# Kernel tuning notes

Hardware: AMD Instinct MI355X
Metric: run time of the kernel (lower is better)

## Reference

```python
import jax, jax.numpy as jnp
import numpy as np

T = 8192      # sequence length (scan steps)
D_IN = 1024   # input feature dim
H = 1024      # d_model (hidden size)


def setup_inputs() -> dict:
    key = jax.random.key(0)
    k1, k2, k3, k4 = jax.random.split(key, 4)
    inputs = jax.random.normal(k1, (T, D_IN), dtype=jnp.float32)
    terminations = jax.random.randint(k2, (T,), 0, 2) > 0  # bool [T]
    last_state = jnp.zeros((H,), dtype=jnp.float32)
    # GRUCell params (flax layout: input kernel with bias for all 3 gates;
    # recurrent kernel, bias only on the candidate 'n' gate).
    # Gate order within the 3H axis: [r, z, n].
    Wi = jax.random.normal(k3, (D_IN, 3 * H), dtype=jnp.float32) / np.sqrt(D_IN)
    bi = jnp.zeros((3 * H,), dtype=jnp.float32)
    Wh = jax.random.normal(k4, (H, 3 * H), dtype=jnp.float32) / np.sqrt(H)
    bhn = jnp.zeros((H,), dtype=jnp.float32)
    return {"inputs": inputs, "terminations": terminations, "last_state": last_state,
            "Wi": Wi, "bi": bi, "Wh": Wh, "bhn": bhn}


def reference(inputs, terminations, last_state, Wi, bi, Wh, bhn):
    # Precompute all input-side gate preactivations in one big GEMM: [T, 3H]
    gi_all = inputs @ Wi + bi

    def step(h, xs):
        gi, term = xs
        # reset_on_terminate: zero the carry when the episode terminated
        h = jnp.where(term, jnp.zeros_like(h), h)
        gh = h @ Wh                      # [3H], recurrent preactivations
        gi_r, gi_z, gi_n = jnp.split(gi, 3)
        gh_r, gh_z, gh_n = jnp.split(gh, 3)
        r = jax.nn.sigmoid(gi_r + gh_r)
        z = jax.nn.sigmoid(gi_z + gh_z)
        n = jnp.tanh(gi_n + r * (gh_n + bhn))
        h_new = (1.0 - z) * n + z * h    # flax GRUCell update
        # GRUout emits (new_c, (new_c, new_h)); flax GRUCell returns new_h twice
        return h_new, (h_new, h_new)

    _, (new_states, y_t) = jax.lax.scan(step, last_state, (gi_all, terminations))
    return (y_t, new_states)  # each [T, H]
```

## Files before the change

### kernel.cpp

```cpp
#include <hip/hip_runtime.h>
#include <stdint.h>

#define T_LEN 8192
#define DIN   1024
#define HD    1024
#define TH    3072
#define NB    16
#define SKINNY_MAX 160
#define KSPLIT 5

typedef __attribute__((ext_vector_type(8))) short bf16x8;
typedef __attribute__((ext_vector_type(4))) float f32x4;

__device__ __forceinline__ unsigned short f2bf(float x) {
    union { float f; unsigned u; } v; v.f = x;
    unsigned r = v.u + 0x7FFFu + ((v.u >> 16) & 1u);
    return (unsigned short)(r >> 16);
}

__device__ __forceinline__ float bf2f(unsigned short x) {
    union { unsigned u; float f; } v; v.u = ((unsigned)x) << 16;
    return v.f;
}

__device__ __forceinline__ void gld16(const void* g, void* l) {
    __builtin_amdgcn_global_load_lds(
        (const __attribute__((address_space(1))) unsigned int*)(uintptr_t)g,
        (__attribute__((address_space(3))) unsigned int*)(uintptr_t)l,
        16, 0, 0);
}

__device__ __forceinline__ float sigm(float x) { return 1.f / (1.f + __expf(-x)); }
__device__ __forceinline__ float tanh_fast(float x) { return 1.f - 2.f / (1.f + __expf(2.f * x)); }

__global__ void cast_x(const float* __restrict__ X, unsigned short* __restrict__ Xb) {
    int idx = (blockIdx.x * 256 + threadIdx.x) * 4;
    float4 v = *(const float4*)(X + idx);
    ushort4 o; o.x = f2bf(v.x); o.y = f2bf(v.y); o.z = f2bf(v.z); o.w = f2bf(v.w);
    *(ushort4*)(Xb + idx) = o;
}

__global__ void transpose_cast(const float* __restrict__ Wi, const float* __restrict__ Wh,
                               unsigned short* __restrict__ WiT, unsigned short* __restrict__ WhT) {
    const float* src = blockIdx.z ? Wh : Wi;
    unsigned short* dst = blockIdx.z ? WhT : WiT;
    int n0 = blockIdx.x * 64, k0 = blockIdx.y * 64;
    __shared__ unsigned short tile[64][65];
    int tid = threadIdx.x;
    for (int p = 0; p < 16; p++) {
        int idx = tid + p * 256;
        int kl = idx >> 6, nl = idx & 63;
        tile[kl][nl] = f2bf(src[(size_t)(k0 + kl) * TH + n0 + nl]);
    }
    __syncthreads();
    for (int p = 0; p < 16; p++) {
        int idx = tid + p * 256;
        int nl = idx >> 6, kl = idx & 63;
        dst[(size_t)(n0 + nl) * 1024 + k0 + kl] = tile[kl][nl];
    }
}

__global__ void meta_kernel(const int* __restrict__ term, const float* __restrict__ last_state,
                            int* __restrict__ pos_list, int* __restrict__ meta) {
    __shared__ int part[1024];
    __shared__ int cnt[NB];
    __shared__ int cur[NB];
    __shared__ int flag;
    int tid = threadIdx.x;
    if (tid < NB) cnt[tid] = 0;
    if (tid == 0) flag = 0;
    __syncthreads();
    int base = tid * 8;
    int mx = -1;
    for (int u = 0; u < 8; u++) {
        int t = base + u;
        int s = (t == 0 || term[t] != 0) ? t : -1;
        mx = s > mx ? s : mx;
    }
    part[tid] = mx;
    __syncthreads();
    for (int d = 1; d < 1024; d <<= 1) {
        int a = part[tid];
        int b = (tid >= d) ? part[tid - d] : -1;
        __syncthreads();
        part[tid] = a > b ? a : b;
        __syncthreads();
    }
    int run = (tid > 0) ? part[tid - 1] : -1;
    int kk[8];
    for (int u = 0; u < 8; u++) {
        int t = base + u;
        int s = (t == 0 || term[t] != 0) ? t : -1;
        run = s > run ? s : run;
        int ls = t - run;
        int k = ls < NB ? ls : NB - 1;
        kk[u] = k;
        atomicAdd(&cnt[k], 1);
    }
    if (last_state[tid] != 0.0f) atomicOr(&flag, 1);
    __syncthreads();
    if (tid == 0) {
        int off = 0;
        for (int k = 0; k < NB; k++) {
            meta[k] = cnt[k];
            meta[NB + k] = off;
            cur[k] = off;
            off += cnt[k];
        }
        meta[2 * NB] = flag;
        meta[48] = 0;
        meta[49] = 0;
    }
    __syncthreads();
    for (int u = 0; u < 8; u++) {
        int idx = atomicAdd(&cur[kk[u]], 1);
        pos_list[idx] = base + u;
    }
}

__global__ __launch_bounds__(256) void gemm_gi(const unsigned short* __restrict__ Xb,
                                               const unsigned short* __restrict__ WiT,
                                               const float* __restrict__ bi,
                                               float* __restrict__ gi) {
    __shared__ unsigned short As[128 * 32];
    __shared__ unsigned short Bs[128 * 32];
    int tid = threadIdx.x;
    int phys = blockIdx.y * gridDim.x + blockIdx.x;
    int logi = (phys & 7) * 192 + (phys >> 3);
    int m0 = (logi / 24) * 128, n0 = (logi % 24) * 128;
    int lane = tid & 63, wave = tid >> 6;
    int wm = wave & 1, wn = wave >> 1;
    int quad = lane >> 4, l16 = lane & 15;
    f32x4 acc[4][4] = {};
    for (int kb = 0; kb < 32; kb++) {
        int k0 = kb * 32;
        for (int p = 0; p < 2; p++) {
            int c = tid + p * 256;
            int row = c >> 2, cb = c & 3;
            gld16(Xb + (size_t)(m0 + row) * 1024 + k0 + cb * 8, As + c * 8);
            gld16(WiT + (size_t)(n0 + row) * 1024 + k0 + cb * 8, Bs + c * 8);
        }
        __syncthreads();
        bf16x8 af[4], bfr[4];
        for (int i = 0; i < 4; i++)
            af[i] = *(const bf16x8*)(As + (wm * 64 + i * 16 + l16) * 32 + quad * 8);
        for (int j = 0; j < 4; j++)
            bfr[j] = *(const bf16x8*)(Bs + (wn * 64 + j * 16 + l16) * 32 + quad * 8);
        for (int i = 0; i < 4; i++)
            for (int j = 0; j < 4; j++)
                acc[i][j] = __builtin_amdgcn_mfma_f32_16x16x32_bf16(af[i], bfr[j], acc[i][j], 0, 0, 0);
        __syncthreads();
    }
    for (int j = 0; j < 4; j++) {
        int col = n0 + wn * 64 + j * 16 + l16;
        float bv = bi[col];
        for (int i = 0; i < 4; i++) {
            int rbase = m0 + wm * 64 + i * 16 + quad * 4;
            for (int r = 0; r < 4; r++)
                gi[(size_t)(rbase + r) * TH + col] = acc[i][j][r] + bv;
        }
    }
}

__global__ void pass0_kernel(const float* __restrict__ gi, const float* __restrict__ bhn,
                             const float* __restrict__ last_state, const float* __restrict__ Wh,
                             const int* __restrict__ term, const int* __restrict__ pos_list,
                             const int* __restrict__ meta, float* __restrict__ out,
                             unsigned short* __restrict__ hb) {
    int S0 = meta[0];
    int b = blockIdx.x;
    if (b >= S0) return;
    int t = pos_list[meta[NB] + b];
    int tid = threadIdx.x;
    bool ls_path = (t == 0) && (term[0] == 0) && (meta[2 * NB] != 0);
    for (int u = 0; u < 4; u++) {
        int j = tid + u * 256;
        float gr = gi[(size_t)t * TH + j];
        float gz = gi[(size_t)t * TH + 1024 + j];
        float gn = gi[(size_t)t * TH + 2048 + j];
        float hp = 0.f, ghr = 0.f, ghz = 0.f, ghn = 0.f;
        if (ls_path) {
            hp = last_state[j];
            for (int k = 0; k < 1024; k++) {
                float hk = last_state[k];
                const float* w = Wh + (size_t)k * TH;
                ghr += hk * w[j]; ghz += hk * w[1024 + j]; ghn += hk * w[2048 + j];
            }
        }
        float r = sigm(gr + ghr);
        float z = sigm(gz + ghz);
        float n = tanh_fast(gn + r * (ghn + bhn[j]));
        float h = (1.f - z) * n + z * hp;
        out[(size_t)t * HD + j] = h;
        out[(size_t)(T_LEN + t) * HD + j] = h;
        hb[(size_t)t * HD + j] = f2bf(h);
    }
}

__global__ __launch_bounds__(256) void pass_gemm(const float* __restrict__ gi,
                                                 const float* __restrict__ bhn,
                                                 const unsigned short* __restrict__ WhT,
                                                 const unsigned short* __restrict__ hb,
                                                 float* __restrict__ out,
                                                 unsigned short* __restrict__ hbw,
                                                 const int* __restrict__ pos_list,
                                                 const int* __restrict__ meta, int k) {
    int S = meta[k];
    int off = meta[NB + k];
    int tid = threadIdx.x;
    int lane = tid & 63, wave = tid >> 6;
    int quad = lane >> 4, l16 = lane & 15;

    if (S <= SKINNY_MAX) {
        if (S == 0) return;
        int nrt = (S + 15) >> 4;
        int ntask = 64 * nrt;
        int gwave = ((blockIdx.y * 16 + blockIdx.x) << 2) + wave;
        int nw = gridDim.x * gridDim.y * 4;
        for (int task = gwave; task < ntask; task += nw) {
            int ct = task & 63;
            int rt = task >> 6;
            int j = ct * 16 + l16;
            int ra = rt * 16 + l16;
            ra = ra < S ? ra : S - 1;
            int t_a = pos_list[off + ra];
            const unsigned short* ap = hb + (size_t)(t_a - 1) * HD + quad * 8;
            const unsigned short* bp = WhT + (size_t)j * 1024 + quad * 8;
            f32x4 acc[3] = {};
            #pragma unroll
            for (int ks = 0; ks < 32; ks++) {
                bf16x8 a  = *(const bf16x8*)(ap + ks * 32);
                bf16x8 b0 = *(const bf16x8*)(bp + ks * 32);
                bf16x8 b1 = *(const bf16x8*)(bp + 1048576 + ks * 32);
                bf16x8 b2 = *(const bf16x8*)(bp + 2097152 + ks * 32);
                acc[0] = __builtin_amdgcn_mfma_f32_16x16x32_bf16(a, b0, acc[0], 0, 0, 0);
                acc[1] = __builtin_amdgcn_mfma_f32_16x16x32_bf16(a, b1, acc[1], 0, 0, 0);
                acc[2] = __builtin_amdgcn_mfma_f32_16x16x32_bf16(a, b2, acc[2], 0, 0, 0);
            }
            #pragma unroll
            for (int r = 0; r < 4; r++) {
                int rr = rt * 16 + quad * 4 + r;
                if (rr >= S) continue;
                int t = pos_list[off + rr];
                const float* girow = gi + (size_t)t * TH;
                float hp = out[(size_t)(t - 1) * HD + j];
                float rgt = sigm(girow[j] + acc[0][r]);
                float zgt = sigm(girow[1024 + j] + acc[1][r]);
                float ngt = tanh_fast(girow[2048 + j] + rgt * (acc[2][r] + bhn[j]));
                float hv = (1.f - zgt) * ngt + zgt * hp;
                out[(size_t)t * HD + j] = hv;
                out[(size_t)(T_LEN + t) * HD + j] = hv;
                hbw[(size_t)t * HD + j] = f2bf(hv);
            }
        }
        return;
    }

    int r0 = blockIdx.y * 64;
    if (r0 >= S) return;
    int j0 = blockIdx.x * 64;
    __shared__ unsigned short As[4 * 64 * 32];
    __shared__ unsigned short Bs[4 * 192 * 32];
    int wm = wave & 1, wn = wave >> 1;

    int arow = tid >> 2, sub = tid & 3;
    bool av = (r0 + arow) < S;
    int t_a = av ? pos_list[off + r0 + arow] : 1;
    const unsigned short* hsrc = hb + (size_t)(t_a - 1) * HD + sub * 8;

    f32x4 acc[2][6] = {};
    for (int kb = 0; kb < 8; kb++) {
        int k0 = kb * 128;
        for (int ks = 0; ks < 4; ks++) {
            int kk0 = k0 + ks * 32;
            for (int p = 0; p < 3; p++) {
                int c = tid + p * 256;
                int row = c >> 2, q = c & 3;
                int g = row >> 6, jj = row & 63;
                gld16(WhT + (size_t)(g * 1024 + j0 + jj) * 1024 + kk0 + q * 8,
                      Bs + ks * 6144 + c * 8);
            }
            gld16(hsrc + kk0, As + ks * 2048 + tid * 8);
        }
        __syncthreads();
        for (int ks = 0; ks < 4; ks++) {
            bf16x8 af[2];
            for (int i = 0; i < 2; i++)
                af[i] = *(const bf16x8*)(As + ks * 2048 + (wm * 32 + i * 16 + l16) * 32 + quad * 8);
            for (int n = 0; n < 6; n++) {
                int g = n >> 1, jh = n & 1;
                bf16x8 bv = *(const bf16x8*)(Bs + ks * 6144 + (g * 64 + wn * 32 + jh * 16 + l16) * 32 + quad * 8);
                for (int i = 0; i < 2; i++)
                    acc[i][n] = __builtin_amdgcn_mfma_f32_16x16x32_bf16(af[i], bv, acc[i][n], 0, 0, 0);
            }
        }
        __syncthreads();
    }
    for (int i = 0; i < 2; i++) {
        for (int r = 0; r < 4; r++) {
            int rr = r0 + wm * 32 + i * 16 + quad * 4 + r;
            if (rr >= S) continue;
            int t = pos_list[off + rr];
            const float* girow = gi + (size_t)t * TH;
            const float* hprow = out + (size_t)(t - 1) * HD;
            float* o1 = out + (size_t)t * HD;
            float* o2 = out + (size_t)(T_LEN + t) * HD;
            unsigned short* hbrow = hbw + (size_t)t * HD;
            for (int jh = 0; jh < 2; jh++) {
                int j = j0 + wn * 32 + jh * 16 + l16;
                float ghr = acc[i][0 + jh][r];
                float ghz = acc[i][2 + jh][r];
                float ghn = acc[i][4 + jh][r];
                float rg = sigm(girow[j] + ghr);
                float zg = sigm(girow[1024 + j] + ghz);
                float ng = tanh_fast(girow[2048 + j] + rg * (ghn + bhn[j]));
                float h = (1.f - zg) * ng + zg * hprow[j];
                o1[j] = h;
                o2[j] = h;
                hbrow[j] = f2bf(h);
            }
        }
    }
}

__global__ __launch_bounds__(256) void skinny_all(const float* __restrict__ gi,
                                                  const float* __restrict__ bhn,
                                                  const unsigned short* __restrict__ WhT,
                                                  unsigned short* __restrict__ hb,
                                                  float* __restrict__ out,
                                                  const int* __restrict__ pos_list,
                                                  const int* __restrict__ meta,
                                                  int* __restrict__ syncc) {
    int tid = threadIdx.x;
    int lane = tid & 63, wave = tid >> 6;
    int quad = lane >> 4, l16 = lane & 15;
    int gwave = (blockIdx.x << 2) + wave;
    int gen = 0;
    for (int k = KSPLIT; k <= NB - 2; k++) {
        int S = meta[k];
        if (S == 0) break;
        int off = meta[NB + k];
        int nrt = (S + 15) >> 4;
        int ntask = 64 * nrt;
        for (int task = gwave; task < ntask; task += 512) {
            int ct = task & 63;
            int rt = task >> 6;
            int j = ct * 16 + l16;
            int ra = rt * 16 + l16;
            ra = ra < S ? ra : S - 1;
            int t_a = pos_list[off + ra];
            const unsigned short* ap = hb + (size_t)(t_a - 1) * HD + quad * 8;
            const unsigned short* bp = WhT + (size_t)j * 1024 + quad * 8;
            f32x4 acc[3] = {};
            #pragma unroll
            for (int ks = 0; ks < 32; ks++) {
                bf16x8 a  = *(const bf16x8*)(ap + ks * 32);
                bf16x8 b0 = *(const bf16x8*)(bp + ks * 32);
                bf16x8 b1 = *(const bf16x8*)(bp + 1048576 + ks * 32);
                bf16x8 b2 = *(const bf16x8*)(bp + 2097152 + ks * 32);
                acc[0] = __builtin_amdgcn_mfma_f32_16x16x32_bf16(a, b0, acc[0], 0, 0, 0);
                acc[1] = __builtin_amdgcn_mfma_f32_16x16x32_bf16(a, b1, acc[1], 0, 0, 0);
                acc[2] = __builtin_amdgcn_mfma_f32_16x16x32_bf16(a, b2, acc[2], 0, 0, 0);
            }
            #pragma unroll
            for (int r = 0; r < 4; r++) {
                int rr = rt * 16 + quad * 4 + r;
                if (rr >= S) continue;
                int t = pos_list[off + rr];
                const float* girow = gi + (size_t)t * TH;
                float hp = out[(size_t)(t - 1) * HD + j];
                float rgt = sigm(girow[j] + acc[0][r]);
                float zgt = sigm(girow[1024 + j] + acc[1][r]);
                float ngt = tanh_fast(girow[2048 + j] + rgt * (acc[2][r] + bhn[j]));
                float hv = (1.f - zgt) * ngt + zgt * hp;
                out[(size_t)t * HD + j] = hv;
                out[(size_t)(T_LEN + t) * HD + j] = hv;
                hb[(size_t)t * HD + j] = f2bf(hv);
            }
        }
        if (k == NB - 2 || meta[k + 1] == 0) break;
        gen++;
        __syncthreads();
        __threadfence();
        if (tid == 0) {
            atomicAdd(syncc, 1);
            while (atomicAdd(syncc, 0) < 128 * gen)
                __builtin_amdgcn_s_sleep(4);
        }
        __syncthreads();
        __threadfence();
    }
}

__global__ __launch_bounds__(256) void tail_pll(const float* __restrict__ gi,
                                                const float* __restrict__ bhn,
                                                const unsigned short* __restrict__ WhT,
                                                const int* __restrict__ pos_list,
                                                const int* __restrict__ meta,
                                                int* __restrict__ sync,
                                                float* __restrict__ out) {
    int S = meta[NB - 1];
    if (S == 0) return;
    __shared__ int pos[T_LEN];
    __shared__ float hsh[HD];
    __shared__ float dots[192];
    int off = meta[NB + NB - 1];
    int tid = threadIdx.x;
    int j0 = blockIdx.x * 64;
    for (int i = tid; i < S; i += 256) pos[i] = pos_list[off + i];
    __syncthreads();
    if (tid == 0) {
        for (int i = 1; i < S; i++) {
            int v = pos[i], j = i - 1;
            while (j >= 0 && pos[j] > v) { pos[j + 1] = pos[j]; j--; }
            pos[j + 1] = v;
        }
    }
    __syncthreads();
    for (int s = 0; s < S; s++) {
        int t = pos[s];
        for (int u = 0; u < 4; u++)
            hsh[tid + u * 256] = out[(size_t)(t - 1) * HD + tid + u * 256];
        __syncthreads();
        if (tid < 192) {
            int g = tid >> 6, jj = tid & 63;
            int col = g * 1024 + j0 + jj;
            const unsigned short* wrow = WhT + (size_t)col * 1024;
            float acc = 0.f;
            for (int kk = 0; kk < 1024; kk += 8) {
                bf16x8 wv = *(const bf16x8*)(wrow + kk);
                f32x4 h0 = *(const f32x4*)(hsh + kk);
                f32x4 h1 = *(const f32x4*)(hsh + kk + 4);
                acc += h0[0] * bf2f((unsigned short)wv[0]) + h0[1] * bf2f((unsigned short)wv[1])
                     + h0[2] * bf2f((unsigned short)wv[2]) + h0[3] * bf2f((unsigned short)wv[3])
                     + h1[0] * bf2f((unsigned short)wv[4]) + h1[1] * bf2f((unsigned short)wv[5])
                     + h1[2] * bf2f((unsigned short)wv[6]) + h1[3] * bf2f((unsigned short)wv[7]);
            }
            dots[tid] = acc;
        }
        __syncthreads();
        if (tid < 64) {
            int j = j0 + tid;
            float rg = sigm(gi[(size_t)t * TH + j] + dots[tid]);
            float zg = sigm(gi[(size_t)t * TH + 1024 + j] + dots[64 + tid]);
            float ng = tanh_fast(gi[(size_t)t * TH + 2048 + j] + rg * (dots[128 + tid] + bhn[j]));
            float hv = (1.f - zg) * ng + zg * hsh[j];
            out[(size_t)t * HD + j] = hv;
            out[(size_t)(T_LEN + t) * HD + j] = hv;
        }
        __threadfence();
        __syncthreads();
        if (tid == 0) {
            atomicAdd(sync, 1);
            int tgt = 16 * (s + 1);
            while (atomicAdd(sync, 0) < tgt)
                __builtin_amdgcn_s_sleep(8);
        }
        __syncthreads();
        __threadfence();
    }
}

extern "C" void kernel_launch(void* const* d_in, const int* in_sizes, int n_in,
                              void* d_out, int out_size, void* d_ws, size_t ws_size,
                              hipStream_t stream) {
    const float* X          = (const float*)d_in[0];
    const int*   term       = (const int*)d_in[1];
    const float* last_state = (const float*)d_in[2];
    const float* Wi         = (const float*)d_in[3];
    const float* bi         = (const float*)d_in[4];
    const float* Wh         = (const float*)d_in[5];
    const float* bhn        = (const float*)d_in[6];
    float* out = (float*)d_out;

    char* ws = (char*)d_ws;
    float*          gi       = (float*)ws;
    unsigned short* Xb       = (unsigned short*)(ws + 100663296);
    unsigned short* hb       = Xb;
    unsigned short* WiT      = (unsigned short*)(ws + 117440512);
    unsigned short* WhT      = (unsigned short*)(ws + 123731968);
    int*            pos_list = (int*)(ws + 130023424);
    int*            meta     = (int*)(ws + 130056192);
    int*            sync_t   = meta + 48;
    int*            sync_s   = meta + 49;

    cast_x<<<dim3(8192), dim3(256), 0, stream>>>(X, Xb);
    transpose_cast<<<dim3(48, 16, 2), dim3(256), 0, stream>>>(Wi, Wh, WiT, WhT);
    meta_kernel<<<dim3(1), dim3(1024), 0, stream>>>(term, last_state, pos_list, meta);
    gemm_gi<<<dim3(24, 64), dim3(256), 0, stream>>>(Xb, WiT, bi, gi);
    pass0_kernel<<<dim3(8192), dim3(256), 0, stream>>>(gi, bhn, last_state, Wh, term, pos_list, meta, out, hb);
    for (int k = 1; k < KSPLIT; k++) {
        int rows_max = T_LEN / (k + 1);
        int gy = (rows_max + 63) / 64;
        pass_gemm<<<dim3(16, gy), dim3(256), 0, stream>>>(gi, bhn, WhT, hb, out, hb, pos_list, meta, k);
    }
    skinny_all<<<dim3(128), dim3(256), 0, stream>>>(gi, bhn, WhT, hb, out, pos_list, meta, sync_s);
    tail_pll<<<dim3(16), dim3(256), 0, stream>>>(gi, bhn, WhT, pos_list, meta, sync_t, out);
}
```

Before: 507.5 us.

## Replace grid barrier in skinny_all with per-timestep dataflow counters

Removes the grid-wide barrier between successive reset-distance levels in the persistent skinny kernel. Each wave now spins on per-timestep completion counters (placed in the WiT workspace, which is dead after the GEMM and is zeroed in pass0) until its predecessor row is fully written, then bumps counters after writing. This lets independent rows of the next level start early instead of waiting for all blocks. The gi GEMM also drops its swizzled block-to-tile mapping in favor of a plain grid mapping, which may change L2 locality.

```diff
diff --git a/kernel.cpp b/kernel.cpp
--- a/kernel.cpp
+++ b/kernel.cpp
@@ -109,7 +109,6 @@
         }
         meta[2 * NB] = flag;
         meta[48] = 0;
-        meta[49] = 0;
     }
     __syncthreads();
     for (int u = 0; u < 8; u++) {
@@ -125,9 +124,7 @@
     __shared__ unsigned short As[128 * 32];
     __shared__ unsigned short Bs[128 * 32];
     int tid = threadIdx.x;
-    int phys = blockIdx.y * gridDim.x + blockIdx.x;
-    int logi = (phys & 7) * 192 + (phys >> 3);
-    int m0 = (logi / 24) * 128, n0 = (logi % 24) * 128;
+    int m0 = blockIdx.y * 128, n0 = blockIdx.x * 128;
     int lane = tid & 63, wave = tid >> 6;
     int wm = wave & 1, wn = wave >> 1;
     int quad = lane >> 4, l16 = lane & 15;
@@ -166,7 +163,8 @@
                              const float* __restrict__ last_state, const float* __restrict__ Wh,
                              const int* __restrict__ term, const int* __restrict__ pos_list,
                              const int* __restrict__ meta, float* __restrict__ out,
-                             unsigned short* __restrict__ hb) {
+                             unsigned short* __restrict__ hb, int* __restrict__ wcnt) {
+    if (blockIdx.x < 32) wcnt[blockIdx.x * 256 + threadIdx.x] = 0;
     int S0 = meta[0];
     int b = blockIdx.x;
     if (b >= S0) return;
@@ -330,12 +328,11 @@
                                                   float* __restrict__ out,
                                                   const int* __restrict__ pos_list,
                                                   const int* __restrict__ meta,
-                                                  int* __restrict__ syncc) {
+                                                  int* __restrict__ wcnt) {
     int tid = threadIdx.x;
     int lane = tid & 63, wave = tid >> 6;
     int quad = lane >> 4, l16 = lane & 15;
     int gwave = (blockIdx.x << 2) + wave;
-    int gen = 0;
     for (int k = KSPLIT; k <= NB - 2; k++) {
         int S = meta[k];
         if (S == 0) break;
@@ -349,6 +346,15 @@
             int ra = rt * 16 + l16;
             ra = ra < S ? ra : S - 1;
             int t_a = pos_list[off + ra];
+            if (k > KSPLIT) {
+                for (;;) {
+                    int c = __hip_atomic_load(&wcnt[t_a - 1], __ATOMIC_RELAXED,
+                                              __HIP_MEMORY_SCOPE_AGENT);
+                    if (__all(c >= 64)) break;
+                    __builtin_amdgcn_s_sleep(1);
+                }
+                __threadfence();
+            }
             const unsigned short* ap = hb + (size_t)(t_a - 1) * HD + quad * 8;
             const unsigned short* bp = WhT + (size_t)j * 1024 + quad * 8;
             f32x4 acc[3] = {};
@@ -377,18 +383,15 @@
                 out[(size_t)(T_LEN + t) * HD + j] = hv;
                 hb[(size_t)t * HD + j] = f2bf(hv);
             }
-        }
-        if (k == NB - 2 || meta[k + 1] == 0) break;
-        gen++;
-        __syncthreads();
-        __threadfence();
-        if (tid == 0) {
-            atomicAdd(syncc, 1);
-            while (atomicAdd(syncc, 0) < 128 * gen)
-                __builtin_amdgcn_s_sleep(4);
-        }
-        __syncthreads();
-        __threadfence();
+            __threadfence();
+            if (l16 == 0) {
+                #pragma unroll
+                for (int r = 0; r < 4; r++) {
+                    int rr = rt * 16 + quad * 4 + r;
+                    if (rr < S) atomicAdd(&wcnt[pos_list[off + rr]], 1);
+                }
+            }
+        }
     }
 }
 
@@ -482,18 +485,18 @@
     int*            pos_list = (int*)(ws + 130023424);
     int*            meta     = (int*)(ws + 130056192);
     int*            sync_t   = meta + 48;
-    int*            sync_s   = meta + 49;
+    int*            wcnt     = (int*)WiT;
 
     cast_x<<<dim3(8192), dim3(256), 0, stream>>>(X, Xb);
     transpose_cast<<<dim3(48, 16, 2), dim3(256), 0, stream>>>(Wi, Wh, WiT, WhT);
     meta_kernel<<<dim3(1), dim3(1024), 0, stream>>>(term, last_state, pos_list, meta);
     gemm_gi<<<dim3(24, 64), dim3(256), 0, stream>>>(Xb, WiT, bi, gi);
-    pass0_kernel<<<dim3(8192), dim3(256), 0, stream>>>(gi, bhn, last_state, Wh, term, pos_list, meta, out, hb);
+    pass0_kernel<<<dim3(8192), dim3(256), 0, stream>>>(gi, bhn, last_state, Wh, term, pos_list, meta, out, hb, wcnt);
     for (int k = 1; k < KSPLIT; k++) {
         int rows_max = T_LEN / (k + 1);
         int gy = (rows_max + 63) / 64;
         pass_gemm<<<dim3(16, gy), dim3(256), 0, stream>>>(gi, bhn, WhT, hb, out, hb, pos_list, meta, k);
     }
-    skinny_all<<<dim3(128), dim3(256), 0, stream>>>(gi, bhn, WhT, hb, out, pos_list, meta, sync_s);
+    skinny_all<<<dim3(128), dim3(256), 0, stream>>>(gi, bhn, WhT, hb, out, pos_list, meta, wcnt);
     tail_pll<<<dim3(16), dim3(256), 0, stream>>>(gi, bhn, WhT, pos_list, meta, sync_t, out);
 }
```

Result: faster. 457.1 us (-9.9%).
